# Performance work log

Measured on AMD Instinct MI355X. Metric: run time of the kernel, lower is better.

Reference implementation:

```python
import jax, jax.numpy as jnp
import numpy as np

B, STEPS, EMB = 2048, 512, 128
HID, CATE = 256, 2
IN_GRU = EMB + STEPS + 1  # input_size + self.length (length+1)


def setup_inputs() -> dict:
    key = jax.random.key(0)
    ks = jax.random.split(key, 7)
    s_ih = 1.0 / np.sqrt(HID)
    inputs = jax.random.normal(ks[0], (B, STEPS, EMB), dtype=jnp.float32)
    W_ih = jax.random.uniform(ks[1], (3 * HID, IN_GRU), jnp.float32, -s_ih, s_ih)
    W_hh = jax.random.uniform(ks[2], (3 * HID, HID), jnp.float32, -s_ih, s_ih)
    b_ih = jax.random.uniform(ks[3], (3 * HID,), jnp.float32, -s_ih, s_ih)
    b_hh = jax.random.uniform(ks[4], (3 * HID,), jnp.float32, -s_ih, s_ih)
    s_cf = 1.0 / np.sqrt(HID)
    W_cf = jax.random.uniform(ks[5], (CATE, HID), jnp.float32, -s_cf, s_cf)
    b_cf = jax.random.uniform(ks[6], (CATE,), jnp.float32, -s_cf, s_cf)
    return {"inputs": inputs, "W_ih": W_ih, "W_hh": W_hh, "b_ih": b_ih,
            "b_hh": b_hh, "W_cf": W_cf, "b_cf": b_cf}


def _gru_cell(x, h, W_ih, W_hh, b_ih, b_hh):
    # torch.nn.GRUCell math: gates ordered (r, z, n)
    gi = x @ W_ih.T + b_ih
    gh = h @ W_hh.T + b_hh
    i_r, i_z, i_n = jnp.split(gi, 3, axis=1)
    h_r, h_z, h_n = jnp.split(gh, 3, axis=1)
    r = jax.nn.sigmoid(i_r + h_r)
    z = jax.nn.sigmoid(i_z + h_z)
    n = jnp.tanh(i_n + r * h_n)
    return (1.0 - z) * n + z * h


def reference(inputs, W_ih, W_hh, b_ih, b_hh, W_cf, b_cf):
    # Eval-mode forward (self.training == False): greedy argmax action.
    b, steps, _ = inputs.shape
    hid = W_hh.shape[1]
    xs = jnp.swapaxes(inputs, 0, 1)  # [steps, b, emb]

    def step(carry, x):
        h, tag = carry
        tag_onehot = jax.nn.one_hot(tag, steps + 1, dtype=x.dtype)  # [b, steps+1]
        i_t = jnp.concatenate([x, tag_onehot], axis=1)
        h = _gru_cell(i_t, h, W_ih, W_hh, b_ih, b_hh)
        probs = jax.nn.softmax(h @ W_cf.T + b_cf, axis=1)  # [b, cate]
        action = jnp.argmax(probs, axis=1)                  # [b]
        pi = jnp.take_along_axis(probs, action[:, None], axis=1)[:, 0]
        tag = tag + action.astype(tag.dtype)  # cumulative sum of actions so far
        return (h, tag), (action.astype(x.dtype), pi)

    h0 = jnp.zeros((b, hid), dtype=inputs.dtype)
    tag0 = jnp.zeros((b,), dtype=jnp.int32)
    _, (outs, pis) = jax.lax.scan(step, (h0, tag0), xs)
    return jnp.swapaxes(outs, 0, 1), jnp.swapaxes(pis, 0, 1)  # each [b, steps]
```

## Files before the change

### kernel.cpp

```cpp
#include <hip/hip_runtime.h>
#include <math.h>

#define BATCH 2048
#define STEPS 512
#define EMB   128
#define HID   256
#define INGRU 641

#define WXP_OFF  49152
#define WCOL_OFF 294912

__global__ void prep_weights(const float* __restrict__ W_ih,
                             const float* __restrict__ W_hh,
                             float* __restrict__ ws) {
    const int idx = blockIdx.x * 256 + threadIdx.x;
    float4* __restrict__ Wp = (float4*)ws;
    if (idx < 49152) {
        const int k4 = idx / 768, rem = idx % 768;
        const int d = rem / 3, g = rem % 3;
        Wp[idx] = *(const float4*)(W_hh + ((size_t)(g * 256 + d)) * HID + 4 * k4);
    }
    if (idx < 24576) {
        const int k4 = idx / 768, rem = idx % 768;
        const int d = rem / 3, g = rem % 3;
        const float* src = W_ih + ((size_t)(g * 256 + d)) * INGRU + 4 * k4;
        Wp[WXP_OFF + idx] = make_float4(src[0], src[1], src[2], src[3]);
    }
    if (idx < 513 * 768) {
        const int c = idx / 768, gg = idx % 768;
        ws[WCOL_OFF + (size_t)c * 768 + gg] = W_ih[(size_t)gg * INGRU + EMB + c];
    }
}

#define FMA8(ACC, S, A, B) do {                                           \
    ACC[0] = fmaf(S, (A).x, ACC[0]); ACC[1] = fmaf(S, (A).y, ACC[1]);     \
    ACC[2] = fmaf(S, (A).z, ACC[2]); ACC[3] = fmaf(S, (A).w, ACC[3]);     \
    ACC[4] = fmaf(S, (B).x, ACC[4]); ACC[5] = fmaf(S, (B).y, ACC[5]);     \
    ACC[6] = fmaf(S, (B).z, ACC[6]); ACC[7] = fmaf(S, (B).w, ACC[7]);     \
} while (0)

#define K1(A0, A1, A2, S0, S1, S2, HP, OFF) do {                          \
    const float4 hA = *(const float4*)((HP) + (OFF));                     \
    const float4 hB = *(const float4*)((HP) + (OFF) + 4);                 \
    FMA8(A0, S0, hA, hB); FMA8(A1, S1, hA, hB); FMA8(A2, S2, hA, hB);     \
} while (0)

#define CONS(A0, A1, A2, W0, W1, W2, HP) do {                             \
    K1(A0, A1, A2, (W0).x, (W1).x, (W2).x, HP, 0);                        \
    K1(A0, A1, A2, (W0).y, (W1).y, (W2).y, HP, 12);                       \
    K1(A0, A1, A2, (W0).z, (W1).z, (W2).z, HP, 24);                       \
    K1(A0, A1, A2, (W0).w, (W1).w, (W2).w, HP, 36);                       \
} while (0)

__global__ __launch_bounds__(512, 2) void gru_policy(
    const float* __restrict__ X,
    const float* __restrict__ ws,
    const float* __restrict__ b_ih,
    const float* __restrict__ b_hh,
    const float* __restrict__ W_cf,
    const float* __restrict__ b_cf,
    float* __restrict__ out)
{
    const float4* __restrict__ Wp   = (const float4*)ws;
    const float*  __restrict__ Wcol = ws + WCOL_OFF;

    __shared__ __align__(16) float h_lds[2][HID][12];
    __shared__ __align__(16) float x_lds[EMB][12];
    __shared__ float ai_lds[3][8][256];
    __shared__ float red[4][8][2];
    __shared__ int   tag_lds[8];

    const int t    = threadIdx.x;
    const int d    = t & 255;
    const int half = t >> 8;
    const int wv   = t >> 6;
    const int lane = t & 63;
    const size_t r0 = (size_t)blockIdx.x * 8;
    const size_t xstride = (size_t)STEPS * EMB;

    const float bc0 = b_cf[0], bc1 = b_cf[1];
    float bh0 = 0.f, bh1 = 0.f, bh2 = 0.f, wcf0 = 0.f, wcf1 = 0.f;
    float bi0 = 0.f, bi1 = 0.f, bi2 = 0.f;
    if (half == 0) {
        bh0 = b_hh[d]; bh1 = b_hh[d + 256]; bh2 = b_hh[d + 512];
        wcf0 = W_cf[d]; wcf1 = W_cf[HID + d];
    } else {
        bi0 = b_ih[d]; bi1 = b_ih[d + 256]; bi2 = b_ih[d + 512];
    }

    if (half == 0) {
        const float4 z4 = make_float4(0.f, 0.f, 0.f, 0.f);
        *(float4*)(&h_lds[0][d][0]) = z4;
        *(float4*)(&h_lds[0][d][4]) = z4;
    } else {
        #pragma unroll
        for (int q = 0; q < 4; ++q) {
            const int i = d + 256 * q, row = i >> 7, col = i & 127;
            x_lds[col][row] = X[(r0 + row) * xstride + col];
        }
    }
    if (t < 8) tag_lds[t] = 0;
    __syncthreads();

    int cur = 0;
    for (int s = 0; s < STEPS; ++s) {
        float aH0[8], aH1[8], aH2[8];
        float xv[4];
        if (half == 0) {
            #pragma unroll
            for (int j = 0; j < 8; ++j) { aH0[j] = bh0; aH1[j] = bh1; aH2[j] = bh2; }
            const float* hb = &h_lds[cur][0][0];
            const float4* wp = Wp + (size_t)d * 3;
            float4 a0 = wp[0], a1 = wp[1], a2 = wp[2]; wp += 768;
            float4 b0 = wp[0], b1 = wp[1], b2 = wp[2]; wp += 768;
            #pragma unroll 2
            for (int it = 0; it < 62; it += 2) {
                const float4 c0 = wp[0], c1 = wp[1], c2 = wp[2]; wp += 768;
                const float4 e0 = wp[0], e1 = wp[1], e2 = wp[2]; wp += 768;
                CONS(aH0, aH1, aH2, a0, a1, a2, hb + it * 48);
                CONS(aH0, aH1, aH2, b0, b1, b2, hb + it * 48 + 48);
                a0 = c0; a1 = c1; a2 = c2; b0 = e0; b1 = e1; b2 = e2;
            }
            CONS(aH0, aH1, aH2, a0, a1, a2, hb + 62 * 48);
            CONS(aH0, aH1, aH2, b0, b1, b2, hb + 63 * 48);
        } else {
            float aI0[8], aI1[8], aI2[8];
            #pragma unroll
            for (int j = 0; j < 8; ++j) {
                const size_t tg = (size_t)tag_lds[j] * 768;
                aI0[j] = bi0 + Wcol[tg + d];
                aI1[j] = bi1 + Wcol[tg + 256 + d];
                aI2[j] = bi2 + Wcol[tg + 512 + d];
            }
            if (s + 1 < STEPS) {
                #pragma unroll
                for (int q = 0; q < 4; ++q) {
                    const int i = d + 256 * q, row = i >> 7, col = i & 127;
                    xv[q] = X[(r0 + row) * xstride + (size_t)(s + 1) * EMB + col];
                }
            }
            const float* xb = &x_lds[0][0];
            const float4* wq = Wp + WXP_OFF + (size_t)d * 3;
            float4 a0 = wq[0], a1 = wq[1], a2 = wq[2]; wq += 768;
            float4 b0 = wq[0], b1 = wq[1], b2 = wq[2]; wq += 768;
            #pragma unroll 2
            for (int it = 0; it < 30; it += 2) {
                const float4 c0 = wq[0], c1 = wq[1], c2 = wq[2]; wq += 768;
                const float4 e0 = wq[0], e1 = wq[1], e2 = wq[2]; wq += 768;
                CONS(aI0, aI1, aI2, a0, a1, a2, xb + it * 48);
                CONS(aI0, aI1, aI2, b0, b1, b2, xb + it * 48 + 48);
                a0 = c0; a1 = c1; a2 = c2; b0 = e0; b1 = e1; b2 = e2;
            }
            CONS(aI0, aI1, aI2, a0, a1, a2, xb + 30 * 48);
            CONS(aI0, aI1, aI2, b0, b1, b2, xb + 31 * 48);
            #pragma unroll
            for (int j = 0; j < 8; ++j) {
                ai_lds[0][j][d] = aI0[j];
                ai_lds[1][j][d] = aI1[j];
                ai_lds[2][j][d] = aI2[j];
            }
        }
        __syncthreads();

        if (half == 0) {
            const float4 hpA = *(const float4*)(&h_lds[cur][d][0]);
            const float4 hpB = *(const float4*)(&h_lds[cur][d][4]);
            const float hpj[8] = {hpA.x, hpA.y, hpA.z, hpA.w,
                                  hpB.x, hpB.y, hpB.z, hpB.w};
            float hn[8], p0[8], p1[8];
            #pragma unroll
            for (int j = 0; j < 8; ++j) {
                const float i0 = ai_lds[0][j][d];
                const float i1 = ai_lds[1][j][d];
                const float i2 = ai_lds[2][j][d];
                const float rr = 1.0f / (1.0f + expf(-(i0 + aH0[j])));
                const float zz = 1.0f / (1.0f + expf(-(i1 + aH1[j])));
                const float nn = tanhf(i2 + rr * aH2[j]);
                const float h  = (1.0f - zz) * nn + zz * hpj[j];
                hn[j] = h;
                p0[j] = h * wcf0;
                p1[j] = h * wcf1;
            }
            *(float4*)(&h_lds[cur ^ 1][d][0]) =
                make_float4(hn[0], hn[1], hn[2], hn[3]);
            *(float4*)(&h_lds[cur ^ 1][d][4]) =
                make_float4(hn[4], hn[5], hn[6], hn[7]);
            #pragma unroll
            for (int m = 32; m >= 1; m >>= 1) {
                #pragma unroll
                for (int j = 0; j < 8; ++j) {
                    p0[j] += __shfl_xor(p0[j], m, 64);
                    p1[j] += __shfl_xor(p1[j], m, 64);
                }
            }
            if (lane == 0) {
                #pragma unroll
                for (int j = 0; j < 8; ++j) {
                    red[wv][j][0] = p0[j];
                    red[wv][j][1] = p1[j];
                }
            }
        } else {
            if (s + 1 < STEPS) {
                #pragma unroll
                for (int q = 0; q < 4; ++q) {
                    const int i = d + 256 * q, row = i >> 7, col = i & 127;
                    x_lds[col][row] = xv[q];
                }
            }
        }
        __syncthreads();

        if (t < 8) {
            float l0 = bc0, l1 = bc1;
            #pragma unroll
            for (int w = 0; w < 4; ++w) {
                l0 += red[w][t][0];
                l1 += red[w][t][1];
            }
            const int act = (l1 > l0) ? 1 : 0;
            const float mx = fmaxf(l0, l1);
            const float e0 = expf(l0 - mx), e1 = expf(l1 - mx);
            const float pi = (act ? e1 : e0) / (e0 + e1);
            const size_t row = r0 + t;
            out[row * STEPS + s] = (float)act;
            out[(size_t)BATCH * STEPS + row * STEPS + s] = pi;
            tag_lds[t] += act;
        }
        __syncthreads();
        cur ^= 1;
    }
}

extern "C" void kernel_launch(void* const* d_in, const int* in_sizes, int n_in,
                              void* d_out, int out_size, void* d_ws, size_t ws_size,
                              hipStream_t stream) {
    const float* X    = (const float*)d_in[0];
    const float* W_ih = (const float*)d_in[1];
    const float* W_hh = (const float*)d_in[2];
    const float* b_ih = (const float*)d_in[3];
    const float* b_hh = (const float*)d_in[4];
    const float* W_cf = (const float*)d_in[5];
    const float* b_cf = (const float*)d_in[6];
    float* out = (float*)d_out;
    float* ws  = (float*)d_ws;

    prep_weights<<<1539, 256, 0, stream>>>(W_ih, W_hh, ws);
    gru_policy<<<BATCH / 8, 512, 0, stream>>>(X, ws, b_ih, b_hh, W_cf, b_cf, out);
}
```

Baseline: 9.243 ms.

## Broadcast hidden state via readlane and move gate math to x-threads

The recurrent matvec now keeps each lane's slice of h in registers and broadcasts values across the wavefront with readlane, instead of reading h from LDS for every FMA. Roles swap so the input-projection threads run the gate nonlinearities and keep h_prev and the tags in registers. Every x-thread recomputes the per-row argmax itself, which drops the final barrier and the tag LDS array. This cuts LDS traffic and one sync per step, but adds many readlane (SALU/VALU) operations and raises register pressure in the hidden-state half.

Measured after the change: 11.56 ms. 25.0% more time.

```diff
diff --git a/kernel.cpp b/kernel.cpp
--- a/kernel.cpp
+++ b/kernel.cpp
@@ -51,6 +51,14 @@
     K1(A0, A1, A2, (W0).z, (W1).z, (W2).z, HP, 24);                       \
     K1(A0, A1, A2, (W0).w, (W1).w, (W2).w, HP, 36);                       \
 } while (0)
+
+__device__ __forceinline__ float bcast_lane(float v, int lane) {
+    return __uint_as_float(
+        __builtin_amdgcn_readlane(__float_as_uint(v), lane));
+}
+__device__ __forceinline__ float f4e(const float4 v, int e) {
+    return e == 0 ? v.x : e == 1 ? v.y : e == 2 ? v.z : v.w;
+}
 
 __global__ __launch_bounds__(512, 2) void gru_policy(
     const float* __restrict__ X,
@@ -64,70 +72,95 @@
     const float4* __restrict__ Wp   = (const float4*)ws;
     const float*  __restrict__ Wcol = ws + WCOL_OFF;
 
-    __shared__ __align__(16) float h_lds[2][HID][12];
+    __shared__ __align__(16) float h2[2][64][33];
     __shared__ __align__(16) float x_lds[EMB][12];
-    __shared__ float ai_lds[3][8][256];
-    __shared__ float red[4][8][2];
-    __shared__ int   tag_lds[8];
-
-    const int t    = threadIdx.x;
-    const int d    = t & 255;
-    const int half = t >> 8;
-    const int wv   = t >> 6;
-    const int lane = t & 63;
+    __shared__ float ah_lds[3][8][256];
+    __shared__ __align__(16) float red[8][8];
+
+    const int t     = threadIdx.x;
+    const int xduty = (t < 256);
+    const int d     = t & 255;
+    const int wv    = t >> 6;
+    const int lane  = t & 63;
     const size_t r0 = (size_t)blockIdx.x * 8;
     const size_t xstride = (size_t)STEPS * EMB;
 
+    const float bh0 = b_hh[d], bh1 = b_hh[d + 256], bh2 = b_hh[d + 512];
+    const float bi0 = b_ih[d], bi1 = b_ih[d + 256], bi2 = b_ih[d + 512];
+    const float wcf0 = W_cf[d], wcf1 = W_cf[256 + d];
     const float bc0 = b_cf[0], bc1 = b_cf[1];
-    float bh0 = 0.f, bh1 = 0.f, bh2 = 0.f, wcf0 = 0.f, wcf1 = 0.f;
-    float bi0 = 0.f, bi1 = 0.f, bi2 = 0.f;
-    if (half == 0) {
-        bh0 = b_hh[d]; bh1 = b_hh[d + 256]; bh2 = b_hh[d + 512];
-        wcf0 = W_cf[d]; wcf1 = W_cf[HID + d];
-    } else {
-        bi0 = b_ih[d]; bi1 = b_ih[d + 256]; bi2 = b_ih[d + 512];
-    }
-
-    if (half == 0) {
-        const float4 z4 = make_float4(0.f, 0.f, 0.f, 0.f);
-        *(float4*)(&h_lds[0][d][0]) = z4;
-        *(float4*)(&h_lds[0][d][4]) = z4;
-    } else {
+
+    int   tags[8];
+    float hp[8];
+    #pragma unroll
+    for (int j = 0; j < 8; ++j) { tags[j] = 0; hp[j] = 0.0f; }
+
+    for (int i = t; i < 64 * 33; i += 512) h2[0][i / 33][i % 33] = 0.0f;
+    if (xduty) {
         #pragma unroll
         for (int q = 0; q < 4; ++q) {
             const int i = d + 256 * q, row = i >> 7, col = i & 127;
             x_lds[col][row] = X[(r0 + row) * xstride + col];
         }
     }
-    if (t < 8) tag_lds[t] = 0;
     __syncthreads();
 
     int cur = 0;
     for (int s = 0; s < STEPS; ++s) {
-        float aH0[8], aH1[8], aH2[8];
-        float xv[4];
-        if (half == 0) {
-            #pragma unroll
-            for (int j = 0; j < 8; ++j) { aH0[j] = bh0; aH1[j] = bh1; aH2[j] = bh2; }
-            const float* hb = &h_lds[cur][0][0];
+        float aI0[8], aI1[8], aI2[8];
+        float xn[4];
+        if (!xduty) {
             const float4* wp = Wp + (size_t)d * 3;
             float4 a0 = wp[0], a1 = wp[1], a2 = wp[2]; wp += 768;
             float4 b0 = wp[0], b1 = wp[1], b2 = wp[2]; wp += 768;
-            #pragma unroll 2
-            for (int it = 0; it < 62; it += 2) {
-                const float4 c0 = wp[0], c1 = wp[1], c2 = wp[2]; wp += 768;
-                const float4 e0 = wp[0], e1 = wp[1], e2 = wp[2]; wp += 768;
-                CONS(aH0, aH1, aH2, a0, a1, a2, hb + it * 48);
-                CONS(aH0, aH1, aH2, b0, b1, b2, hb + it * 48 + 48);
-                a0 = c0; a1 = c1; a2 = c2; b0 = e0; b1 = e1; b2 = e2;
-            }
-            CONS(aH0, aH1, aH2, a0, a1, a2, hb + 62 * 48);
-            CONS(aH0, aH1, aH2, b0, b1, b2, hb + 63 * 48);
+
+            float hreg[32];
+            #pragma unroll
+            for (int m = 0; m < 32; ++m) hreg[m] = h2[cur][lane][m];
+
+            float aH0[8], aH1[8], aH2[8];
+            #pragma unroll
+            for (int j = 0; j < 8; ++j) { aH0[j] = bh0; aH1[j] = bh1; aH2[j] = bh2; }
+
+            __builtin_amdgcn_s_setprio(1);
+            #pragma unroll 1
+            for (int kb = 0; kb < 8; ++kb) {
+                const int lb = kb << 3;
+                #pragma unroll
+                for (int m4 = 0; m4 < 8; ++m4) {
+                    float4 w0, w1, w2;
+                    if ((m4 & 1) == 0) {
+                        w0 = a0; w1 = a1; w2 = a2;
+                        a0 = wp[0]; a1 = wp[1]; a2 = wp[2]; wp += 768;
+                    } else {
+                        w0 = b0; w1 = b1; w2 = b2;
+                        b0 = wp[0]; b1 = wp[1]; b2 = wp[2]; wp += 768;
+                    }
+                    #pragma unroll
+                    for (int e = 0; e < 4; ++e) {
+                        const float we0 = f4e(w0, e), we1 = f4e(w1, e), we2 = f4e(w2, e);
+                        const int rm = (m4 << 2) | e;
+                        #pragma unroll
+                        for (int j = 0; j < 8; ++j) {
+                            const float sv = bcast_lane(hreg[rm], lb + j);
+                            aH0[j] = fmaf(we0, sv, aH0[j]);
+                            aH1[j] = fmaf(we1, sv, aH1[j]);
+                            aH2[j] = fmaf(we2, sv, aH2[j]);
+                        }
+                    }
+                }
+            }
+            __builtin_amdgcn_s_setprio(0);
+            #pragma unroll
+            for (int j = 0; j < 8; ++j) {
+                ah_lds[0][j][d] = aH0[j];
+                ah_lds[1][j][d] = aH1[j];
+                ah_lds[2][j][d] = aH2[j];
+            }
         } else {
-            float aI0[8], aI1[8], aI2[8];
-            #pragma unroll
-            for (int j = 0; j < 8; ++j) {
-                const size_t tg = (size_t)tag_lds[j] * 768;
+            #pragma unroll
+            for (int j = 0; j < 8; ++j) {
+                const size_t tg = (size_t)tags[j] * 768;
                 aI0[j] = bi0 + Wcol[tg + d];
                 aI1[j] = bi1 + Wcol[tg + 256 + d];
                 aI2[j] = bi2 + Wcol[tg + 512 + d];
@@ -136,7 +169,7 @@
                 #pragma unroll
                 for (int q = 0; q < 4; ++q) {
                     const int i = d + 256 * q, row = i >> 7, col = i & 127;
-                    xv[q] = X[(r0 + row) * xstride + (size_t)(s + 1) * EMB + col];
+                    xn[q] = X[(r0 + row) * xstride + (size_t)(s + 1) * EMB + col];
                 }
             }
             const float* xb = &x_lds[0][0];
@@ -153,38 +186,25 @@
             }
             CONS(aI0, aI1, aI2, a0, a1, a2, xb + 30 * 48);
             CONS(aI0, aI1, aI2, b0, b1, b2, xb + 31 * 48);
-            #pragma unroll
-            for (int j = 0; j < 8; ++j) {
-                ai_lds[0][j][d] = aI0[j];
-                ai_lds[1][j][d] = aI1[j];
-                ai_lds[2][j][d] = aI2[j];
-            }
         }
         __syncthreads();
 
-        if (half == 0) {
-            const float4 hpA = *(const float4*)(&h_lds[cur][d][0]);
-            const float4 hpB = *(const float4*)(&h_lds[cur][d][4]);
-            const float hpj[8] = {hpA.x, hpA.y, hpA.z, hpA.w,
-                                  hpB.x, hpB.y, hpB.z, hpB.w};
-            float hn[8], p0[8], p1[8];
-            #pragma unroll
-            for (int j = 0; j < 8; ++j) {
-                const float i0 = ai_lds[0][j][d];
-                const float i1 = ai_lds[1][j][d];
-                const float i2 = ai_lds[2][j][d];
-                const float rr = 1.0f / (1.0f + expf(-(i0 + aH0[j])));
-                const float zz = 1.0f / (1.0f + expf(-(i1 + aH1[j])));
-                const float nn = tanhf(i2 + rr * aH2[j]);
-                const float h  = (1.0f - zz) * nn + zz * hpj[j];
-                hn[j] = h;
+        if (xduty) {
+            float p0[8], p1[8];
+            #pragma unroll
+            for (int j = 0; j < 8; ++j) {
+                const float ah0 = ah_lds[0][j][d];
+                const float ah1 = ah_lds[1][j][d];
+                const float ah2 = ah_lds[2][j][d];
+                const float rr = 1.0f / (1.0f + expf(-(aI0[j] + ah0)));
+                const float zz = 1.0f / (1.0f + expf(-(aI1[j] + ah1)));
+                const float nn = tanhf(aI2[j] + rr * ah2);
+                const float h  = (1.0f - zz) * nn + zz * hp[j];
+                hp[j] = h;
+                h2[cur ^ 1][((d >> 5) << 3) | j][d & 31] = h;
                 p0[j] = h * wcf0;
                 p1[j] = h * wcf1;
             }
-            *(float4*)(&h_lds[cur ^ 1][d][0]) =
-                make_float4(hn[0], hn[1], hn[2], hn[3]);
-            *(float4*)(&h_lds[cur ^ 1][d][4]) =
-                make_float4(hn[4], hn[5], hn[6], hn[7]);
             #pragma unroll
             for (int m = 32; m >= 1; m >>= 1) {
                 #pragma unroll
@@ -196,38 +216,39 @@
             if (lane == 0) {
                 #pragma unroll
                 for (int j = 0; j < 8; ++j) {
-                    red[wv][j][0] = p0[j];
-                    red[wv][j][1] = p1[j];
-                }
-            }
-        } else {
+                    red[j][wv * 2]     = p0[j];
+                    red[j][wv * 2 + 1] = p1[j];
+                }
+            }
             if (s + 1 < STEPS) {
                 #pragma unroll
                 for (int q = 0; q < 4; ++q) {
                     const int i = d + 256 * q, row = i >> 7, col = i & 127;
-                    x_lds[col][row] = xv[q];
+                    x_lds[col][row] = xn[q];
                 }
             }
         }
         __syncthreads();
 
-        if (t < 8) {
-            float l0 = bc0, l1 = bc1;
-            #pragma unroll
-            for (int w = 0; w < 4; ++w) {
-                l0 += red[w][t][0];
-                l1 += red[w][t][1];
-            }
-            const int act = (l1 > l0) ? 1 : 0;
-            const float mx = fmaxf(l0, l1);
-            const float e0 = expf(l0 - mx), e1 = expf(l1 - mx);
-            const float pi = (act ? e1 : e0) / (e0 + e1);
-            const size_t row = r0 + t;
-            out[row * STEPS + s] = (float)act;
-            out[(size_t)BATCH * STEPS + row * STEPS + s] = pi;
-            tag_lds[t] += act;
-        }
-        __syncthreads();
+        if (xduty) {
+            #pragma unroll
+            for (int j = 0; j < 8; ++j) {
+                const float4 rA = *(const float4*)&red[j][0];
+                const float4 rB = *(const float4*)&red[j][4];
+                float l0 = bc0; l0 += rA.x; l0 += rA.z; l0 += rB.x; l0 += rB.z;
+                float l1 = bc1; l1 += rA.y; l1 += rA.w; l1 += rB.y; l1 += rB.w;
+                const int act = (l1 > l0) ? 1 : 0;
+                tags[j] += act;
+                if (t == j) {
+                    const float mx = fmaxf(l0, l1);
+                    const float e0 = expf(l0 - mx), e1 = expf(l1 - mx);
+                    const float pi = (act ? e1 : e0) / (e0 + e1);
+                    const size_t row = r0 + j;
+                    out[row * STEPS + s] = (float)act;
+                    out[(size_t)BATCH * STEPS + row * STEPS + s] = pi;
+                }
+            }
+        }
         cur ^= 1;
     }
 }
```

## Deepen weight prefetch to four-slot ring buffer and raise priority of recurrent GEMV

Applied to the files above, without the earlier changes.

Replaces the two-deep register double-buffer of streamed weight float4s with a four-slot rotating buffer in both the recurrent (h) and input (x) matvec loops. This keeps more global/L2 weight loads in flight to hide latency. It also raises wave priority with s_setprio around the recurrent half, since that half is on the per-step critical path. The cost is more VGPRs under launch_bounds(512,2), which risks spilling, and unroll 1 adds loop overhead.

Measured after the change: 9.757 ms. 5.6% more time.

```diff
diff --git a/kernel.cpp b/kernel.cpp
--- a/kernel.cpp
+++ b/kernel.cpp
@@ -50,6 +50,16 @@
     K1(A0, A1, A2, (W0).y, (W1).y, (W2).y, HP, 12);                       \
     K1(A0, A1, A2, (W0).z, (W1).z, (W2).z, HP, 24);                       \
     K1(A0, A1, A2, (W0).w, (W1).w, (W2).w, HP, 36);                       \
+} while (0)
+
+#define SLOT4(A0, A1, A2, Q) do {                                         \
+    const float4 u0 = wb[Q][0], u1 = wb[Q][1], u2 = wb[Q][2];             \
+    wb[Q][0] = wp[0]; wb[Q][1] = wp[1]; wb[Q][2] = wp[2]; wp += 768;      \
+    CONS(A0, A1, A2, u0, u1, u2, hb); hb += 48;                           \
+} while (0)
+
+#define SLOTE(A0, A1, A2, Q) do {                                         \
+    CONS(A0, A1, A2, wb[Q][0], wb[Q][1], wb[Q][2], hb); hb += 48;         \
 } while (0)
 
 __global__ __launch_bounds__(512, 2) void gru_policy(
@@ -111,18 +121,24 @@
             for (int j = 0; j < 8; ++j) { aH0[j] = bh0; aH1[j] = bh1; aH2[j] = bh2; }
             const float* hb = &h_lds[cur][0][0];
             const float4* wp = Wp + (size_t)d * 3;
-            float4 a0 = wp[0], a1 = wp[1], a2 = wp[2]; wp += 768;
-            float4 b0 = wp[0], b1 = wp[1], b2 = wp[2]; wp += 768;
-            #pragma unroll 2
-            for (int it = 0; it < 62; it += 2) {
-                const float4 c0 = wp[0], c1 = wp[1], c2 = wp[2]; wp += 768;
-                const float4 e0 = wp[0], e1 = wp[1], e2 = wp[2]; wp += 768;
-                CONS(aH0, aH1, aH2, a0, a1, a2, hb + it * 48);
-                CONS(aH0, aH1, aH2, b0, b1, b2, hb + it * 48 + 48);
-                a0 = c0; a1 = c1; a2 = c2; b0 = e0; b1 = e1; b2 = e2;
-            }
-            CONS(aH0, aH1, aH2, a0, a1, a2, hb + 62 * 48);
-            CONS(aH0, aH1, aH2, b0, b1, b2, hb + 63 * 48);
+            float4 wb[4][3];
+            #pragma unroll
+            for (int q = 0; q < 4; ++q) {
+                wb[q][0] = wp[0]; wb[q][1] = wp[1]; wb[q][2] = wp[2]; wp += 768;
+            }
+            __builtin_amdgcn_s_setprio(1);
+            #pragma unroll 1
+            for (int it = 0; it < 15; ++it) {
+                SLOT4(aH0, aH1, aH2, 0);
+                SLOT4(aH0, aH1, aH2, 1);
+                SLOT4(aH0, aH1, aH2, 2);
+                SLOT4(aH0, aH1, aH2, 3);
+            }
+            SLOTE(aH0, aH1, aH2, 0);
+            SLOTE(aH0, aH1, aH2, 1);
+            SLOTE(aH0, aH1, aH2, 2);
+            SLOTE(aH0, aH1, aH2, 3);
+            __builtin_amdgcn_s_setprio(0);
         } else {
             float aI0[8], aI1[8], aI2[8];
             #pragma unroll
@@ -139,20 +155,24 @@
                     xv[q] = X[(r0 + row) * xstride + (size_t)(s + 1) * EMB + col];
                 }
             }
-            const float* xb = &x_lds[0][0];
-            const float4* wq = Wp + WXP_OFF + (size_t)d * 3;
-            float4 a0 = wq[0], a1 = wq[1], a2 = wq[2]; wq += 768;
-            float4 b0 = wq[0], b1 = wq[1], b2 = wq[2]; wq += 768;
-            #pragma unroll 2
-            for (int it = 0; it < 30; it += 2) {
-                const float4 c0 = wq[0], c1 = wq[1], c2 = wq[2]; wq += 768;
-                const float4 e0 = wq[0], e1 = wq[1], e2 = wq[2]; wq += 768;
-                CONS(aI0, aI1, aI2, a0, a1, a2, xb + it * 48);
-                CONS(aI0, aI1, aI2, b0, b1, b2, xb + it * 48 + 48);
-                a0 = c0; a1 = c1; a2 = c2; b0 = e0; b1 = e1; b2 = e2;
-            }
-            CONS(aI0, aI1, aI2, a0, a1, a2, xb + 30 * 48);
-            CONS(aI0, aI1, aI2, b0, b1, b2, xb + 31 * 48);
+            const float* hb = &x_lds[0][0];
+            const float4* wp = Wp + WXP_OFF + (size_t)d * 3;
+            float4 wb[4][3];
+            #pragma unroll
+            for (int q = 0; q < 4; ++q) {
+                wb[q][0] = wp[0]; wb[q][1] = wp[1]; wb[q][2] = wp[2]; wp += 768;
+            }
+            #pragma unroll 1
+            for (int it = 0; it < 7; ++it) {
+                SLOT4(aI0, aI1, aI2, 0);
+                SLOT4(aI0, aI1, aI2, 1);
+                SLOT4(aI0, aI1, aI2, 2);
+                SLOT4(aI0, aI1, aI2, 3);
+            }
+            SLOTE(aI0, aI1, aI2, 0);
+            SLOTE(aI0, aI1, aI2, 1);
+            SLOTE(aI0, aI1, aI2, 2);
+            SLOTE(aI0, aI1, aI2, 3);
             #pragma unroll
             for (int j = 0; j < 8; ++j) {
                 ai_lds[0][j][d] = aI0[j];
```
